# Kernel tuning notes

Measured on AMD Instinct MI355X. Metric: run time of the kernel, lower is better.

The kernel has to match this reference:

```python
import jax, jax.numpy as jnp
import numpy as np

H, D_MODEL, D_K, D_V = 16, 1024, 64, 64
B, L = 4, 2048

def _linear_params(key, in_dim, out_dim):
    kw, kb = jax.random.split(key)
    bound = 1.0 / np.sqrt(in_dim)
    W = jax.random.uniform(kw, (out_dim, in_dim), jnp.float32, -bound, bound)
    b = jax.random.uniform(kb, (out_dim,), jnp.float32, -bound, bound)
    return W, b

def setup_inputs() -> dict:
    key = jax.random.key(0)
    ks = jax.random.split(key, 7)
    V = jax.random.normal(ks[0], (B, L, D_MODEL), jnp.float32)
    K = jax.random.normal(ks[1], (B, L, D_MODEL), jnp.float32)
    Q = jax.random.normal(ks[2], (B, L, D_MODEL), jnp.float32)
    Wv, bv = _linear_params(ks[3], D_MODEL, H * D_V)
    Wk, bk = _linear_params(ks[4], D_MODEL, H * D_K)
    Wq, bq = _linear_params(ks[5], D_MODEL, H * D_K)
    Wo, bo = _linear_params(ks[6], H * D_V, D_MODEL)
    return {"V": V, "K": K, "Q": Q, "Wv": Wv, "bv": bv, "Wk": Wk, "bk": bk,
            "Wq": Wq, "bq": bq, "Wo": Wo, "bo": bo}

def reference(V, K, Q, Wv, bv, Wk, bk, Wq, bq, Wo, bo):
    batch, len1, _ = V.shape
    len2 = Q.shape[1]
    # project and split heads: (b, l, h, d)
    v = (V @ Wv.T + bv).reshape(batch, len1, H, D_V)
    k = (K @ Wk.T + bk).reshape(batch, len1, H, D_K)
    q = (Q @ Wq.T + bq).reshape(batch, len2, H, D_K)
    scale = 1.0 / jnp.sqrt(jnp.asarray(D_K, q.dtype))
    # scores: (b, h, len2, len1)
    scores = jnp.einsum('bqhd,bkhd->bhqk', q, k) * scale
    attn = jax.nn.softmax(scores, axis=-1)
    out = jnp.einsum('bhqk,bkhd->bqhd', attn, v).reshape(batch, len2, H * D_V)
    return out @ Wo.T + bo
```

## Files before the change

### kernel.cpp

```cpp
#include <hip/hip_runtime.h>


typedef __bf16 bf16;
typedef __attribute__((ext_vector_type(8))) __bf16 bf16x8;
typedef __attribute__((ext_vector_type(4))) __bf16 bf16x4;
typedef __attribute__((ext_vector_type(4))) float f32x4;
typedef __attribute__((ext_vector_type(16))) float f32x16;

__global__ __launch_bounds__(256) void cvt_all(
    const float* __restrict__ Q, const float* __restrict__ K, const float* __restrict__ V,
    const float* __restrict__ Wq, const float* __restrict__ Wk,
    const float* __restrict__ Wv, const float* __restrict__ Wo,
    bf16* __restrict__ ws)
{
    int bid = blockIdx.x;
    const float* src;
    bf16* dst;
    int lb;
    if (bid < 4096)       { src = Q;  dst = ws;             lb = bid; }
    else if (bid < 8192)  { src = K;  dst = ws + 8388608;   lb = bid - 4096; }
    else if (bid < 12288) { src = V;  dst = ws + 16777216;  lb = bid - 8192; }
    else if (bid < 12800) { src = Wq; dst = ws + 25165824;  lb = bid - 12288; }
    else if (bid < 13312) { src = Wk; dst = ws + 26214400;  lb = bid - 12800; }
    else if (bid < 13824) { src = Wv; dst = ws + 27262976;  lb = bid - 13312; }
    else                  { src = Wo; dst = ws + 28311552;  lb = bid - 13824; }
    size_t i = ((size_t)lb * 256 + threadIdx.x) * 8;
    f32x4 a = *(const f32x4*)(src + i);
    f32x4 b = *(const f32x4*)(src + i + 4);
    bf16x8 o;
    o[0] = (bf16)a[0]; o[1] = (bf16)a[1]; o[2] = (bf16)a[2]; o[3] = (bf16)a[3];
    o[4] = (bf16)b[0]; o[5] = (bf16)b[1]; o[6] = (bf16)b[2]; o[7] = (bf16)b[3];
    *(bf16x8*)(dst + i) = o;
}

__device__ inline void gld_lds16(const void* g, void* l) {
    __builtin_amdgcn_global_load_lds((const __attribute__((address_space(1))) void*)g,
                                     (__attribute__((address_space(3))) void*)l, 16, 0, 0);
}

__device__ inline int swz4(int r) { return (r & 3) ^ ((r >> 2) & 3); }

__global__ __launch_bounds__(256) void proj_fused(
    const bf16* __restrict__ Xq, const bf16* __restrict__ Xk, const bf16* __restrict__ Xv,
    const bf16* __restrict__ Wqb, const bf16* __restrict__ Wkb, const bf16* __restrict__ Wvb,
    const float* __restrict__ bq, const float* __restrict__ bk, const float* __restrict__ bv,
    bf16* __restrict__ qw, bf16* __restrict__ kw, bf16* __restrict__ vtw)
{
    __shared__ bf16 lA[3][4096];
    __shared__ bf16 lB[3][4096];
    const int z = blockIdx.z;
    const bf16*  A    = z == 0 ? Xq  : (z == 1 ? Xk  : Xv);
    const bf16*  W    = z == 0 ? Wqb : (z == 1 ? Wkb : Wvb);
    const float* bias = z == 0 ? bq  : (z == 1 ? bk  : bv);
    bf16*        out  = z == 0 ? qw  : (z == 1 ? kw  : vtw);
    const float scale = z == 0 ? 0.18033688011112042f : 1.0f;

    const int tid  = threadIdx.x;
    const int wave = tid >> 6, lane = tid & 63;
    const int c = lane & 15, g = lane >> 4;

    const int oid = blockIdx.y * 8 + blockIdx.x;
    const int nid = (oid & 7) * 64 + (oid >> 3);
    const int m0 = (nid >> 3) * 128, n0 = (nid & 7) * 128;

    const int wr = wave >> 1, wc = wave & 1;
    const int srow  = lane >> 2;
    const int sscol = (((lane & 3) ^ swz4(srow)) * 8);
    const int rdsw  = (g ^ swz4(c)) * 8;

    f32x4 acc[4][4] = {};

#define PSTAGE(kt_, bb)                                                         \
    {                                                                           \
        _Pragma("unroll")                                                       \
        for (int h = 0; h < 2; ++h) {                                           \
            int ca = wave + h * 4;                                              \
            int arow = ca * 16 + srow;                                          \
            gld_lds16(A + (size_t)(m0 + arow) * 1024 + (kt_) * 32 + sscol,      \
                      &lA[bb][ca * 512]);                                       \
            gld_lds16(W + (size_t)(n0 + arow) * 1024 + (kt_) * 32 + sscol,      \
                      &lB[bb][ca * 512]);                                       \
        }                                                                       \
    }

    PSTAGE(0, 0);
    PSTAGE(1, 1);

    for (int kt = 0; kt < 32; ++kt) {
        const int buf = kt % 3;
        if (kt + 2 < 32) {
            PSTAGE(kt + 2, (kt + 2) % 3);
            asm volatile("s_waitcnt vmcnt(8)" ::: "memory");
        } else if (kt + 2 == 32) {
            asm volatile("s_waitcnt vmcnt(4)" ::: "memory");
        } else {
            asm volatile("s_waitcnt vmcnt(0)" ::: "memory");
        }
        __builtin_amdgcn_s_barrier();
        asm volatile("" ::: "memory");

        bf16x8 af[4], bfr[4];
#pragma unroll
        for (int m = 0; m < 4; ++m)
            af[m] = *(const bf16x8*)&lA[buf][(wr * 4 + m) * 512 + c * 32 + rdsw];
#pragma unroll
        for (int n = 0; n < 4; ++n)
            bfr[n] = *(const bf16x8*)&lB[buf][(wc * 4 + n) * 512 + c * 32 + rdsw];
#pragma unroll
        for (int m = 0; m < 4; ++m)
#pragma unroll
            for (int n = 0; n < 4; ++n)
                acc[m][n] = __builtin_amdgcn_mfma_f32_16x16x32_bf16(af[m], bfr[n], acc[m][n], 0, 0, 0);

        asm volatile("" ::: "memory");
        __builtin_amdgcn_s_barrier();
        asm volatile("" ::: "memory");
    }
#undef PSTAGE

#pragma unroll
    for (int m = 0; m < 4; ++m) {
#pragma unroll
        for (int n = 0; n < 4; ++n) {
            int col  = n0 + wc * 64 + n * 16 + c;
            float bb = bias[col];
#pragma unroll
            for (int r = 0; r < 4; ++r) {
                int row = m0 + wr * 64 + m * 16 + 4 * g + r;
                float v = (acc[m][n][r] + bb) * scale;
                int b = row >> 11, l = row & 2047, hh = col >> 6, d = col & 63;
                size_t base = (size_t)(b * 16 + hh) * 131072;
                if (z < 2) {
                    out[base + (l >> 5) * 2048 + (d >> 4) * 512 +
                        ((d >> 3) & 1) * 256 + (l & 31) * 8 + (d & 7)] = (bf16)v;
                } else {
                    out[base + (l >> 5) * 2048 + (d >> 5) * 1024 +
                        ((l >> 4) & 1) * 512 + ((l >> 3) & 1) * 256 +
                        (d & 31) * 8 + (l & 7)] = (bf16)v;
                }
            }
        }
    }
}

__global__ __launch_bounds__(256) void gemm_out(
    const bf16* __restrict__ A, const bf16* __restrict__ W,
    const float* __restrict__ bias, float* __restrict__ out)
{
    __shared__ bf16 lA[3][4096];
    __shared__ bf16 lB[3][4096];
    const int tid  = threadIdx.x;
    const int wave = tid >> 6, lane = tid & 63;
    const int c = lane & 15, g = lane >> 4;

    const int oid = blockIdx.y * 8 + blockIdx.x;
    const int nid = (oid & 7) * 64 + (oid >> 3);
    const int m0 = (nid >> 3) * 128, n0 = (nid & 7) * 128;

    const int wr = wave >> 1, wc = wave & 1;
    const int srow  = lane >> 2;
    const int sscol = (((lane & 3) ^ swz4(srow)) * 8);
    const int rdsw  = (g ^ swz4(c)) * 8;

    f32x4 acc[4][4] = {};

#define OSTAGE(kt_, bb)                                                         \
    {                                                                           \
        _Pragma("unroll")                                                       \
        for (int h = 0; h < 2; ++h) {                                           \
            int ca = wave + h * 4;                                              \
            int arow = ca * 16 + srow;                                          \
            gld_lds16(A + (size_t)(m0 + arow) * 1024 + (kt_) * 32 + sscol,      \
                      &lA[bb][ca * 512]);                                       \
            gld_lds16(W + (size_t)(n0 + arow) * 1024 + (kt_) * 32 + sscol,      \
                      &lB[bb][ca * 512]);                                       \
        }                                                                       \
    }

    OSTAGE(0, 0);
    OSTAGE(1, 1);

    for (int kt = 0; kt < 32; ++kt) {
        const int buf = kt % 3;
        if (kt + 2 < 32) {
            OSTAGE(kt + 2, (kt + 2) % 3);
            asm volatile("s_waitcnt vmcnt(8)" ::: "memory");
        } else if (kt + 2 == 32) {
            asm volatile("s_waitcnt vmcnt(4)" ::: "memory");
        } else {
            asm volatile("s_waitcnt vmcnt(0)" ::: "memory");
        }
        __builtin_amdgcn_s_barrier();
        asm volatile("" ::: "memory");

        bf16x8 af[4], bfr[4];
#pragma unroll
        for (int m = 0; m < 4; ++m)
            af[m] = *(const bf16x8*)&lA[buf][(wr * 4 + m) * 512 + c * 32 + rdsw];
#pragma unroll
        for (int n = 0; n < 4; ++n)
            bfr[n] = *(const bf16x8*)&lB[buf][(wc * 4 + n) * 512 + c * 32 + rdsw];
#pragma unroll
        for (int m = 0; m < 4; ++m)
#pragma unroll
            for (int n = 0; n < 4; ++n)
                acc[m][n] = __builtin_amdgcn_mfma_f32_16x16x32_bf16(af[m], bfr[n], acc[m][n], 0, 0, 0);

        asm volatile("" ::: "memory");
        __builtin_amdgcn_s_barrier();
        asm volatile("" ::: "memory");
    }
#undef OSTAGE

#pragma unroll
    for (int m = 0; m < 4; ++m) {
#pragma unroll
        for (int n = 0; n < 4; ++n) {
            int col  = n0 + wc * 64 + n * 16 + c;
            float bb = bias[col];
#pragma unroll
            for (int r = 0; r < 4; ++r) {
                int row = m0 + wr * 64 + m * 16 + 4 * g + r;
                out[(size_t)row * 1024 + col] = acc[m][n][r] + bb;
            }
        }
    }
}

__device__ inline unsigned cvtpk(float lo, float hi) {
    unsigned r;
    asm("v_cvt_pk_bf16_f32 %0, %1, %2" : "=v"(r) : "v"(lo), "v"(hi));
    return r;
}
__device__ inline void pswap(unsigned &a, unsigned &b) {
    asm("v_permlane32_swap_b32 %0, %1" : "+v"(a), "+v"(b));
}

__global__ __launch_bounds__(512) void attn_kernel(
    const bf16* __restrict__ q, const bf16* __restrict__ k,
    const bf16* __restrict__ vt, bf16* __restrict__ O)
{
    __shared__ bf16 lkv[3][4096];
    const int tid  = threadIdx.x;
    const int wave = tid >> 6, lane = tid & 63;
    const int l31 = lane & 31, hi = lane >> 5;
    const int orig = blockIdx.x;
    const int swz  = (orig & 7) * 64 + (orig >> 3);
    const int bh = swz >> 3;
    const int q0 = (swz & 7) * 256 + wave * 32;
    const int laneoff = hi * 256 + l31 * 8;

    const bf16* qb = q  + (size_t)bh * 131072 + (q0 >> 5) * 2048 + laneoff;
    const bf16* kb = k  + (size_t)bh * 131072;
    const bf16* vb = vt + (size_t)bh * 131072;

    bf16x8 qf0 = *(const bf16x8*)(qb);
    bf16x8 qf1 = *(const bf16x8*)(qb + 512);
    bf16x8 qf2 = *(const bf16x8*)(qb + 1024);
    bf16x8 qf3 = *(const bf16x8*)(qb + 1536);

    const bf16* sg = (wave < 4) ? (kb + wave * 512 + lane * 8)
                                : (vb + (wave - 4) * 512 + lane * 8);
    const int   sl = (wave < 4) ? wave * 512 : 2048 + (wave - 4) * 512;

    bf16x8 ones;
#pragma unroll
    for (int i = 0; i < 8; ++i) ones[i] = (bf16)1.0f;

    f32x16 acc0 = {}, acc1 = {}, accS = {};

    gld_lds16(sg,        &lkv[0][sl]);
    gld_lds16(sg + 2048, &lkv[1][sl]);

    int cur = 0;
    for (int t = 0; t < 64; ++t) {
        if (t < 62) {
            int nb = cur + 2; if (nb >= 3) nb -= 3;
            gld_lds16(sg + (size_t)(t + 2) * 2048, &lkv[nb][sl]);
            asm volatile("s_waitcnt vmcnt(2)" ::: "memory");
        } else if (t == 62) {
            asm volatile("s_waitcnt vmcnt(1)" ::: "memory");
        } else {
            asm volatile("s_waitcnt vmcnt(0)" ::: "memory");
        }
        __syncthreads();

        const bf16* kl = &lkv[cur][laneoff];
        const bf16* vl = &lkv[cur][2048 + laneoff];
        bf16x8 kf0  = *(const bf16x8*)(kl);
        bf16x8 kf1  = *(const bf16x8*)(kl + 512);
        bf16x8 kf2  = *(const bf16x8*)(kl + 1024);
        bf16x8 kf3  = *(const bf16x8*)(kl + 1536);
        bf16x8 vf00 = *(const bf16x8*)(vl);
        bf16x8 vf01 = *(const bf16x8*)(vl + 512);
        bf16x8 vf10 = *(const bf16x8*)(vl + 1024);
        bf16x8 vf11 = *(const bf16x8*)(vl + 1536);

        f32x16 st = {};
        __builtin_amdgcn_s_setprio(1);
        st = __builtin_amdgcn_mfma_f32_32x32x16_bf16(kf0, qf0, st, 0, 0, 0);
        st = __builtin_amdgcn_mfma_f32_32x32x16_bf16(kf1, qf1, st, 0, 0, 0);
        st = __builtin_amdgcn_mfma_f32_32x32x16_bf16(kf2, qf2, st, 0, 0, 0);
        st = __builtin_amdgcn_mfma_f32_32x32x16_bf16(kf3, qf3, st, 0, 0, 0);
        __builtin_amdgcn_s_setprio(0);

#pragma unroll
        for (int r = 0; r < 16; ++r) st[r] = __builtin_amdgcn_exp2f(st[r]);

        unsigned u01 = cvtpk(st[0],  st[1]),  u23 = cvtpk(st[2],  st[3]);
        unsigned u45 = cvtpk(st[4],  st[5]),  u67 = cvtpk(st[6],  st[7]);
        unsigned u89 = cvtpk(st[8],  st[9]),  uAB = cvtpk(st[10], st[11]);
        unsigned uCD = cvtpk(st[12], st[13]), uEF = cvtpk(st[14], st[15]);
        pswap(u01, u45); pswap(u23, u67);
        pswap(u89, uCD); pswap(uAB, uEF);
        union { unsigned u[4]; bf16x8 v; } pf0, pf1;
        pf0.u[0] = u01; pf0.u[1] = u23; pf0.u[2] = u45; pf0.u[3] = u67;
        pf1.u[0] = u89; pf1.u[1] = uAB; pf1.u[2] = uCD; pf1.u[3] = uEF;

        __builtin_amdgcn_s_setprio(1);
        acc0 = __builtin_amdgcn_mfma_f32_32x32x16_bf16(vf00, pf0.v, acc0, 0, 0, 0);
        acc1 = __builtin_amdgcn_mfma_f32_32x32x16_bf16(vf10, pf0.v, acc1, 0, 0, 0);
        accS = __builtin_amdgcn_mfma_f32_32x32x16_bf16(ones, pf0.v, accS, 0, 0, 0);
        acc0 = __builtin_amdgcn_mfma_f32_32x32x16_bf16(vf01, pf1.v, acc0, 0, 0, 0);
        acc1 = __builtin_amdgcn_mfma_f32_32x32x16_bf16(vf11, pf1.v, acc1, 0, 0, 0);
        accS = __builtin_amdgcn_mfma_f32_32x32x16_bf16(ones, pf1.v, accS, 0, 0, 0);
        __builtin_amdgcn_s_setprio(0);

        __syncthreads();
        cur = (cur == 2) ? 0 : cur + 1;
    }

    float inv = 1.0f / accS[0];
    int qg = q0 + l31;
    bf16* ob = O + ((size_t)(bh >> 4) * 2048 + qg) * 1024 + (size_t)(bh & 15) * 64;
#pragma unroll
    for (int rg = 0; rg < 4; ++rg) {
        bf16x4 w0, w1;
#pragma unroll
        for (int i = 0; i < 4; ++i) {
            w0[i] = (bf16)(acc0[rg * 4 + i] * inv);
            w1[i] = (bf16)(acc1[rg * 4 + i] * inv);
        }
        *(bf16x4*)(ob + 8 * rg + 4 * hi)      = w0;
        *(bf16x4*)(ob + 32 + 8 * rg + 4 * hi) = w1;
    }
}

extern "C" void kernel_launch(void* const* d_in, const int* in_sizes, int n_in,
                              void* d_out, int out_size, void* d_ws, size_t ws_size,
                              hipStream_t stream) {
    (void)in_sizes; (void)n_in; (void)out_size; (void)ws_size;
    const float* V  = (const float*)d_in[0];
    const float* K  = (const float*)d_in[1];
    const float* Q  = (const float*)d_in[2];
    const float* Wv = (const float*)d_in[3];
    const float* bv = (const float*)d_in[4];
    const float* Wk = (const float*)d_in[5];
    const float* bk = (const float*)d_in[6];
    const float* Wq = (const float*)d_in[7];
    const float* bq = (const float*)d_in[8];
    const float* Wo = (const float*)d_in[9];
    const float* bo = (const float*)d_in[10];

    char* ws = (char*)d_ws;
    const size_t MB = 1ull << 20;
    bf16* Xq  = (bf16*)(ws + 0);
    bf16* Xk  = (bf16*)(ws + 16 * MB);
    bf16* Xv  = (bf16*)(ws + 32 * MB);
    bf16* Wqb = (bf16*)(ws + 48 * MB);
    bf16* Wkb = (bf16*)(ws + 50 * MB);
    bf16* Wvb = (bf16*)(ws + 52 * MB);
    bf16* Wob = (bf16*)(ws + 54 * MB);
    bf16* qw  = (bf16*)(ws + 56 * MB);
    bf16* kw  = (bf16*)(ws + 72 * MB);
    bf16* vtw = (bf16*)(ws + 88 * MB);
    bf16* Ow  = (bf16*)(ws + 0);

    cvt_all<<<14336, 256, 0, stream>>>(Q, K, V, Wq, Wk, Wv, Wo, (bf16*)ws);

    proj_fused<<<dim3(8, 64, 3), 256, 0, stream>>>(
        Xq, Xk, Xv, Wqb, Wkb, Wvb, bq, bk, bv, qw, kw, vtw);

    attn_kernel<<<512, 512, 0, stream>>>(qw, kw, vtw, Ow);

    gemm_out<<<dim3(8, 64), 256, 0, stream>>>(Ow, Wob, bo, (float*)d_out);
}
```

Measured before the change: 200.3 us.

## Use BK=64 double-buffered K tiles with XOR-8 swizzle in projection GEMMs

Both the fused QKV projection and the output projection GEMMs switch from a triple-buffered 32-wide K tile to a double-buffered 64-wide K tile with an 8-way XOR swizzle. Each iteration now runs two MFMA k-substeps per barrier pair, halving the number of barriers and loop iterations. Prefetch of stage kt+2 moves after the end-of-iteration barrier into the buffer just consumed. The catch is less lookahead, since the prefetch is issued after compute, and LDS use grows from 48KB to 64KB per block, which may lower occupancy.

```diff
diff --git a/kernel.cpp b/kernel.cpp
--- a/kernel.cpp
+++ b/kernel.cpp
@@ -38,16 +38,14 @@
                                      (__attribute__((address_space(3))) void*)l, 16, 0, 0);
 }
 
-__device__ inline int swz4(int r) { return (r & 3) ^ ((r >> 2) & 3); }
-
 __global__ __launch_bounds__(256) void proj_fused(
     const bf16* __restrict__ Xq, const bf16* __restrict__ Xk, const bf16* __restrict__ Xv,
     const bf16* __restrict__ Wqb, const bf16* __restrict__ Wkb, const bf16* __restrict__ Wvb,
     const float* __restrict__ bq, const float* __restrict__ bk, const float* __restrict__ bv,
     bf16* __restrict__ qw, bf16* __restrict__ kw, bf16* __restrict__ vtw)
 {
-    __shared__ bf16 lA[3][4096];
-    __shared__ bf16 lB[3][4096];
+    __shared__ bf16 lA[2][8192];
+    __shared__ bf16 lB[2][8192];
     const int z = blockIdx.z;
     const bf16*  A    = z == 0 ? Xq  : (z == 1 ? Xk  : Xv);
     const bf16*  W    = z == 0 ? Wqb : (z == 1 ? Wkb : Wvb);
@@ -64,21 +62,21 @@
     const int m0 = (nid >> 3) * 128, n0 = (nid & 7) * 128;
 
     const int wr = wave >> 1, wc = wave & 1;
-    const int srow  = lane >> 2;
-    const int sscol = (((lane & 3) ^ swz4(srow)) * 8);
-    const int rdsw  = (g ^ swz4(c)) * 8;
+    const int srow  = lane >> 3;
+    const int scol8 = ((lane & 7) ^ srow) * 8;
+    const int c7 = c & 7;
 
     f32x4 acc[4][4] = {};
 
 #define PSTAGE(kt_, bb)                                                         \
     {                                                                           \
         _Pragma("unroll")                                                       \
-        for (int h = 0; h < 2; ++h) {                                           \
-            int ca = wave + h * 4;                                              \
-            int arow = ca * 16 + srow;                                          \
-            gld_lds16(A + (size_t)(m0 + arow) * 1024 + (kt_) * 32 + sscol,      \
+        for (int i = 0; i < 4; ++i) {                                           \
+            int ca = wave * 4 + i;                                              \
+            int arow = ca * 8 + srow;                                           \
+            gld_lds16(A + (size_t)(m0 + arow) * 1024 + (kt_) * 64 + scol8,      \
                       &lA[bb][ca * 512]);                                       \
-            gld_lds16(W + (size_t)(n0 + arow) * 1024 + (kt_) * 32 + sscol,      \
+            gld_lds16(W + (size_t)(n0 + arow) * 1024 + (kt_) * 64 + scol8,      \
                       &lB[bb][ca * 512]);                                       \
         }                                                                       \
     }
@@ -86,35 +84,40 @@
     PSTAGE(0, 0);
     PSTAGE(1, 1);
 
-    for (int kt = 0; kt < 32; ++kt) {
-        const int buf = kt % 3;
-        if (kt + 2 < 32) {
-            PSTAGE(kt + 2, (kt + 2) % 3);
+    for (int kt = 0; kt < 16; ++kt) {
+        const int buf = kt & 1;
+        if (kt < 15) {
             asm volatile("s_waitcnt vmcnt(8)" ::: "memory");
-        } else if (kt + 2 == 32) {
-            asm volatile("s_waitcnt vmcnt(4)" ::: "memory");
         } else {
             asm volatile("s_waitcnt vmcnt(0)" ::: "memory");
         }
         __builtin_amdgcn_s_barrier();
         asm volatile("" ::: "memory");
 
-        bf16x8 af[4], bfr[4];
-#pragma unroll
-        for (int m = 0; m < 4; ++m)
-            af[m] = *(const bf16x8*)&lA[buf][(wr * 4 + m) * 512 + c * 32 + rdsw];
-#pragma unroll
-        for (int n = 0; n < 4; ++n)
-            bfr[n] = *(const bf16x8*)&lB[buf][(wc * 4 + n) * 512 + c * 32 + rdsw];
-#pragma unroll
-        for (int m = 0; m < 4; ++m)
-#pragma unroll
-            for (int n = 0; n < 4; ++n)
-                acc[m][n] = __builtin_amdgcn_mfma_f32_16x16x32_bf16(af[m], bfr[n], acc[m][n], 0, 0, 0);
+#pragma unroll
+        for (int ks = 0; ks < 2; ++ks) {
+            bf16x8 af[4], bfr[4];
+#pragma unroll
+            for (int m = 0; m < 4; ++m) {
+                int r = wr * 64 + m * 16 + c;
+                af[m] = *(const bf16x8*)&lA[buf][r * 64 + (((ks * 4 + g) ^ c7) * 8)];
+            }
+#pragma unroll
+            for (int n = 0; n < 4; ++n) {
+                int r = wc * 64 + n * 16 + c;
+                bfr[n] = *(const bf16x8*)&lB[buf][r * 64 + (((ks * 4 + g) ^ c7) * 8)];
+            }
+#pragma unroll
+            for (int m = 0; m < 4; ++m)
+#pragma unroll
+                for (int n = 0; n < 4; ++n)
+                    acc[m][n] = __builtin_amdgcn_mfma_f32_16x16x32_bf16(af[m], bfr[n], acc[m][n], 0, 0, 0);
+        }
 
         asm volatile("" ::: "memory");
         __builtin_amdgcn_s_barrier();
         asm volatile("" ::: "memory");
+        if (kt + 2 < 16) PSTAGE(kt + 2, buf);
     }
 #undef PSTAGE
 
@@ -147,8 +150,8 @@
     const bf16* __restrict__ A, const bf16* __restrict__ W,
     const float* __restrict__ bias, float* __restrict__ out)
 {
-    __shared__ bf16 lA[3][4096];
-    __shared__ bf16 lB[3][4096];
+    __shared__ bf16 lA[2][8192];
+    __shared__ bf16 lB[2][8192];
     const int tid  = threadIdx.x;
     const int wave = tid >> 6, lane = tid & 63;
     const int c = lane & 15, g = lane >> 4;
@@ -158,21 +161,21 @@
     const int m0 = (nid >> 3) * 128, n0 = (nid & 7) * 128;
 
     const int wr = wave >> 1, wc = wave & 1;
-    const int srow  = lane >> 2;
-    const int sscol = (((lane & 3) ^ swz4(srow)) * 8);
-    const int rdsw  = (g ^ swz4(c)) * 8;
+    const int srow  = lane >> 3;
+    const int scol8 = ((lane & 7) ^ srow) * 8;
+    const int c7 = c & 7;
 
     f32x4 acc[4][4] = {};
 
 #define OSTAGE(kt_, bb)                                                         \
     {                                                                           \
         _Pragma("unroll")                                                       \
-        for (int h = 0; h < 2; ++h) {                                           \
-            int ca = wave + h * 4;                                              \
-            int arow = ca * 16 + srow;                                          \
-            gld_lds16(A + (size_t)(m0 + arow) * 1024 + (kt_) * 32 + sscol,      \
+        for (int i = 0; i < 4; ++i) {                                           \
+            int ca = wave * 4 + i;                                              \
+            int arow = ca * 8 + srow;                                           \
+            gld_lds16(A + (size_t)(m0 + arow) * 1024 + (kt_) * 64 + scol8,      \
                       &lA[bb][ca * 512]);                                       \
-            gld_lds16(W + (size_t)(n0 + arow) * 1024 + (kt_) * 32 + sscol,      \
+            gld_lds16(W + (size_t)(n0 + arow) * 1024 + (kt_) * 64 + scol8,      \
                       &lB[bb][ca * 512]);                                       \
         }                                                                       \
     }
@@ -180,35 +183,40 @@
     OSTAGE(0, 0);
     OSTAGE(1, 1);
 
-    for (int kt = 0; kt < 32; ++kt) {
-        const int buf = kt % 3;
-        if (kt + 2 < 32) {
-            OSTAGE(kt + 2, (kt + 2) % 3);
+    for (int kt = 0; kt < 16; ++kt) {
+        const int buf = kt & 1;
+        if (kt < 15) {
             asm volatile("s_waitcnt vmcnt(8)" ::: "memory");
-        } else if (kt + 2 == 32) {
-            asm volatile("s_waitcnt vmcnt(4)" ::: "memory");
         } else {
             asm volatile("s_waitcnt vmcnt(0)" ::: "memory");
         }
         __builtin_amdgcn_s_barrier();
         asm volatile("" ::: "memory");
 
-        bf16x8 af[4], bfr[4];
-#pragma unroll
-        for (int m = 0; m < 4; ++m)
-            af[m] = *(const bf16x8*)&lA[buf][(wr * 4 + m) * 512 + c * 32 + rdsw];
-#pragma unroll
-        for (int n = 0; n < 4; ++n)
-            bfr[n] = *(const bf16x8*)&lB[buf][(wc * 4 + n) * 512 + c * 32 + rdsw];
-#pragma unroll
-        for (int m = 0; m < 4; ++m)
-#pragma unroll
-            for (int n = 0; n < 4; ++n)
-                acc[m][n] = __builtin_amdgcn_mfma_f32_16x16x32_bf16(af[m], bfr[n], acc[m][n], 0, 0, 0);
+#pragma unroll
+        for (int ks = 0; ks < 2; ++ks) {
+            bf16x8 af[4], bfr[4];
+#pragma unroll
+            for (int m = 0; m < 4; ++m) {
+                int r = wr * 64 + m * 16 + c;
+                af[m] = *(const bf16x8*)&lA[buf][r * 64 + (((ks * 4 + g) ^ c7) * 8)];
+            }
+#pragma unroll
+            for (int n = 0; n < 4; ++n) {
+                int r = wc * 64 + n * 16 + c;
+                bfr[n] = *(const bf16x8*)&lB[buf][r * 64 + (((ks * 4 + g) ^ c7) * 8)];
+            }
+#pragma unroll
+            for (int m = 0; m < 4; ++m)
+#pragma unroll
+                for (int n = 0; n < 4; ++n)
+                    acc[m][n] = __builtin_amdgcn_mfma_f32_16x16x32_bf16(af[m], bfr[n], acc[m][n], 0, 0, 0);
+        }
 
         asm volatile("" ::: "memory");
         __builtin_amdgcn_s_barrier();
         asm volatile("" ::: "memory");
+        if (kt + 2 < 16) OSTAGE(kt + 2, buf);
     }
 #undef OSTAGE
 
```

New measurement: 187.7 us. -6.3%, faster.
